# Performance work log

Hardware: AMD Instinct MI355X
Metric: run time of the kernel (lower is better)

## Reference

```python
import jax, jax.numpy as jnp
import numpy as np

N, C_IN, H, W = 16, 32, 512, 512
C_OUT, K, STRIDE = 32, 3, 1


def setup_inputs() -> dict:
    key = jax.random.key(0)
    k1, k2, k3 = jax.random.split(key, 3)
    x = jax.random.normal(k1, (N, C_IN, H, W), dtype=jnp.float32)
    weight = jax.random.normal(k2, (C_OUT, C_IN, K, K), dtype=jnp.float32) * 0.05
    bias = jax.random.normal(k3, (C_OUT,), dtype=jnp.float32) * 0.05
    return {"x": x, "weight": weight, "bias": bias}


def reference(x, weight, bias):
    # Direct 2D convolution, NCHW / OIHW, stride 1, no padding (VALID),
    # matching the module's per-pixel multiply+sum with padding=0.
    out = jax.lax.conv_general_dilated(
        x, weight,
        window_strides=(STRIDE, STRIDE),
        padding="VALID",
        dimension_numbers=("NCHW", "OIHW", "NCHW"),
    )
    return out + bias[None, :, None, None]
```

## Files before the change

### kernel.cpp

```cpp
#include <hip/hip_runtime.h>


namespace {
constexpr int NI    = 16;
constexpr int C_IN  = 32;
constexpr int HI    = 512;
constexpr int WI    = 512;
constexpr int C_OUT = 32;
constexpr int HO    = 510;
constexpr int WO    = 510;

constexpr int RT    = 6;
constexpr int PT    = 64;
constexpr int XROWS = RT + 2;
constexpr int XCOLS = PT + 2;
constexpr int PSTR  = 36;
constexpr int HIWI  = HI * WI;
}

typedef __attribute__((ext_vector_type(4))) float  floatx4;
typedef __attribute__((ext_vector_type(8))) __bf16 bf16x8;
typedef __attribute__((ext_vector_type(4))) __bf16 bf16x4;
typedef __attribute__((ext_vector_type(4))) unsigned short ushortx4;

__global__ void conv_wprep(const float* __restrict__ w, __bf16* __restrict__ ws) {
  const int t = threadIdx.x;
  for (int i = t; i < 9 * 2 * 64 * 8; i += 256) {
    const int j    = i & 7;
    const int lane = (i >> 3) & 63;
    const int h    = (i >> 9) & 1;
    const int tap  = i >> 10;
    const int co   = h * 16 + (lane & 15);
    const int ci   = (lane >> 4) * 8 + j;
    ws[i] = (__bf16)w[(co * C_IN + ci) * 9 + tap];
  }
}

__global__ __launch_bounds__(256, 4)
void conv3x3_mfma(const float* __restrict__ x, const __bf16* __restrict__ ws,
                  const float* __restrict__ bias, float* __restrict__ out) {
  __shared__ unsigned short lds[XROWS * XCOLS * PSTR];

  const int t    = threadIdx.x;
  const int lane = t & 63;
  const int wv   = t >> 6;
  const int quad = lane >> 4;
  const int l16  = lane & 15;

  const int x0 = blockIdx.x * PT;
  const int y0 = blockIdx.y * RT;
  const int n  = blockIdx.z;

  for (int p = t; p < XROWS * XCOLS; p += 256) {
    const int row = p / XCOLS;
    const int col = p - row * XCOLS;
    int gx = x0 + col;
    if (gx > WI - 1) gx = WI - 1;
    const float* xp = x + ((size_t)(n * C_IN) * HI + (y0 + row)) * WI + gx;
    union { __bf16 b[32]; ushortx4 q[8]; } pk;
#pragma unroll
    for (int ci = 0; ci < C_IN; ++ci)
      pk.b[ci] = (__bf16)xp[ci * HIWI];
    unsigned short* dst = &lds[p * PSTR];
#pragma unroll
    for (int k = 0; k < 8; ++k)
      *reinterpret_cast<ushortx4*>(dst + k * 4) = pk.q[k];
  }

  bf16x8 afrag[9][2];
#pragma unroll
  for (int tap = 0; tap < 9; ++tap)
#pragma unroll
    for (int h = 0; h < 2; ++h)
      afrag[tap][h] = *reinterpret_cast<const bf16x8*>(ws + ((tap * 2 + h) * 64 + lane) * 8);

  float b0[4], b1[4];
#pragma unroll
  for (int r = 0; r < 4; ++r) {
    b0[r] = bias[quad * 4 + r];
    b1[r] = bias[quad * 4 + r + 16];
  }

  __syncthreads();

  const int pbase  = wv * 16 + l16;
  const int px     = x0 + pbase;
  const bool valid = px < WO;

  for (int row = 0; row < RT; ++row) {
    floatx4 acc0 = {b0[0], b0[1], b0[2], b0[3]};
    floatx4 acc1 = {b1[0], b1[1], b1[2], b1[3]};
#pragma unroll
    for (int ky = 0; ky < 3; ++ky)
#pragma unroll
      for (int kx = 0; kx < 3; ++kx) {
        union { bf16x8 v; bf16x4 h[2]; } bf;
        const int base = ((row + ky) * XCOLS + pbase + kx) * PSTR + quad * 8;
        bf.h[0] = *reinterpret_cast<const bf16x4*>(&lds[base]);
        bf.h[1] = *reinterpret_cast<const bf16x4*>(&lds[base + 4]);
        acc0 = __builtin_amdgcn_mfma_f32_16x16x32_bf16(afrag[ky * 3 + kx][0], bf.v, acc0, 0, 0, 0);
        acc1 = __builtin_amdgcn_mfma_f32_16x16x32_bf16(afrag[ky * 3 + kx][1], bf.v, acc1, 0, 0, 0);
      }
    if (valid) {
      float* op = out + ((size_t)(n * C_OUT + quad * 4) * HO + (y0 + row)) * WO + px;
#pragma unroll
      for (int r = 0; r < 4; ++r) {
        op[r * (HO * WO)]        = acc0[r];
        op[(16 + r) * (HO * WO)] = acc1[r];
      }
    }
  }
}

extern "C" void kernel_launch(void* const* d_in, const int* in_sizes, int n_in,
                              void* d_out, int out_size, void* d_ws, size_t ws_size,
                              hipStream_t stream) {
  const float* x    = (const float*)d_in[0];
  const float* w    = (const float*)d_in[1];
  const float* bias = (const float*)d_in[2];
  float* out        = (float*)d_out;
  __bf16* ws        = (__bf16*)d_ws;

  conv_wprep<<<dim3(1), 256, 0, stream>>>(w, ws);

  dim3 grid(WI / PT, HO / RT, NI);
  conv3x3_mfma<<<grid, 256, 0, stream>>>(x, ws, bias, out);
}
```

Measured before the change: 1.001 ms.

## Split waves across output-channel halves and halve row tile for occupancy

Each wave now computes 16 output channels for 32 pixels instead of 32 channels for 16 pixels. This halves the per-wave A-fragment registers, and the launch bound is raised to allow more resident blocks. The row tile drops from 6 to 3, which shrinks LDS per block but raises the halo overhead (5 input rows loaded per 3 output rows) and doubles the number of blocks. Each wave also issues twice the B-fragment LDS reads per MFMA pair while reusing each A fragment twice.

```diff
diff --git a/kernel.cpp b/kernel.cpp
--- a/kernel.cpp
+++ b/kernel.cpp
@@ -10,7 +10,7 @@
 constexpr int HO    = 510;
 constexpr int WO    = 510;
 
-constexpr int RT    = 6;
+constexpr int RT    = 3;
 constexpr int PT    = 64;
 constexpr int XROWS = RT + 2;
 constexpr int XCOLS = PT + 2;
@@ -36,7 +36,7 @@
   }
 }
 
-__global__ __launch_bounds__(256, 4)
+__global__ __launch_bounds__(256, 6)
 void conv3x3_mfma(const float* __restrict__ x, const __bf16* __restrict__ ws,
                   const float* __restrict__ bias, float* __restrict__ out) {
   __shared__ unsigned short lds[XROWS * XCOLS * PSTR];
@@ -46,6 +46,8 @@
   const int wv   = t >> 6;
   const int quad = lane >> 4;
   const int l16  = lane & 15;
+  const int xh   = wv & 1;
+  const int ch   = wv >> 1;
 
   const int x0 = blockIdx.x * PT;
   const int y0 = blockIdx.y * RT;
@@ -67,47 +69,44 @@
       *reinterpret_cast<ushortx4*>(dst + k * 4) = pk.q[k];
   }
 
-  bf16x8 afrag[9][2];
+  bf16x8 afrag[9];
 #pragma unroll
   for (int tap = 0; tap < 9; ++tap)
+    afrag[tap] = *reinterpret_cast<const bf16x8*>(ws + ((tap * 2 + ch) * 64 + lane) * 8);
+
+  float bv[4];
 #pragma unroll
-    for (int h = 0; h < 2; ++h)
-      afrag[tap][h] = *reinterpret_cast<const bf16x8*>(ws + ((tap * 2 + h) * 64 + lane) * 8);
-
-  float b0[4], b1[4];
-#pragma unroll
-  for (int r = 0; r < 4; ++r) {
-    b0[r] = bias[quad * 4 + r];
-    b1[r] = bias[quad * 4 + r + 16];
-  }
+  for (int r = 0; r < 4; ++r)
+    bv[r] = bias[ch * 16 + quad * 4 + r];
 
   __syncthreads();
 
-  const int pbase  = wv * 16 + l16;
-  const int px     = x0 + pbase;
-  const bool valid = px < WO;
+  const int p0  = xh * 32 + l16;
+  const int px0 = x0 + p0;
+  const int px1 = px0 + 16;
+  const bool valid1 = px1 < WO;
 
   for (int row = 0; row < RT; ++row) {
-    floatx4 acc0 = {b0[0], b0[1], b0[2], b0[3]};
-    floatx4 acc1 = {b1[0], b1[1], b1[2], b1[3]};
+    floatx4 acc0 = {bv[0], bv[1], bv[2], bv[3]};
+    floatx4 acc1 = {bv[0], bv[1], bv[2], bv[3]};
 #pragma unroll
     for (int ky = 0; ky < 3; ++ky)
 #pragma unroll
       for (int kx = 0; kx < 3; ++kx) {
-        union { bf16x8 v; bf16x4 h[2]; } bf;
-        const int base = ((row + ky) * XCOLS + pbase + kx) * PSTR + quad * 8;
-        bf.h[0] = *reinterpret_cast<const bf16x4*>(&lds[base]);
-        bf.h[1] = *reinterpret_cast<const bf16x4*>(&lds[base + 4]);
-        acc0 = __builtin_amdgcn_mfma_f32_16x16x32_bf16(afrag[ky * 3 + kx][0], bf.v, acc0, 0, 0, 0);
-        acc1 = __builtin_amdgcn_mfma_f32_16x16x32_bf16(afrag[ky * 3 + kx][1], bf.v, acc1, 0, 0, 0);
+        const int base0 = ((row + ky) * XCOLS + p0 + kx) * PSTR + quad * 8;
+        union { bf16x8 v; bf16x4 h[2]; } bf0, bf1;
+        bf0.h[0] = *reinterpret_cast<const bf16x4*>(&lds[base0]);
+        bf0.h[1] = *reinterpret_cast<const bf16x4*>(&lds[base0 + 4]);
+        bf1.h[0] = *reinterpret_cast<const bf16x4*>(&lds[base0 + 16 * PSTR]);
+        bf1.h[1] = *reinterpret_cast<const bf16x4*>(&lds[base0 + 16 * PSTR + 4]);
+        acc0 = __builtin_amdgcn_mfma_f32_16x16x32_bf16(afrag[ky * 3 + kx], bf0.v, acc0, 0, 0, 0);
+        acc1 = __builtin_amdgcn_mfma_f32_16x16x32_bf16(afrag[ky * 3 + kx], bf1.v, acc1, 0, 0, 0);
       }
-    if (valid) {
-      float* op = out + ((size_t)(n * C_OUT + quad * 4) * HO + (y0 + row)) * WO + px;
+    float* op = out + ((size_t)(n * C_OUT + ch * 16 + quad * 4) * HO + (y0 + row)) * WO;
 #pragma unroll
-      for (int r = 0; r < 4; ++r) {
-        op[r * (HO * WO)]        = acc0[r];
-        op[(16 + r) * (HO * WO)] = acc1[r];
-      }
+    for (int r = 0; r < 4; ++r) {
+      op[r * (HO * WO) + px0] = acc0[r];
+      if (valid1) op[r * (HO * WO) + px1] = acc1[r];
     }
   }
 }
```

After: 1.420 ms. 41.8% more time.

## Split output channels across twice as many waves per block

Applied to the files above, without the earlier changes.

Doubles the block to 512 threads, so each wave computes 16 output channels for its 16-pixel strip instead of all 32. The LDS tile load is spread over more threads and each wave holds half the weight fragments, which lowers register pressure and adds waves for latency hiding. In exchange, each wave now reads the input fragments from LDS for only one MFMA, doubling LDS reads per MFMA.

```diff
diff --git a/kernel.cpp b/kernel.cpp
--- a/kernel.cpp
+++ b/kernel.cpp
@@ -16,6 +16,7 @@
 constexpr int XCOLS = PT + 2;
 constexpr int PSTR  = 36;
 constexpr int HIWI  = HI * WI;
+constexpr int NT    = 512;
 }
 
 typedef __attribute__((ext_vector_type(4))) float  floatx4;
@@ -36,7 +37,7 @@
   }
 }
 
-__global__ __launch_bounds__(256, 4)
+__global__ __launch_bounds__(NT, 8)
 void conv3x3_mfma(const float* __restrict__ x, const __bf16* __restrict__ ws,
                   const float* __restrict__ bias, float* __restrict__ out) {
   __shared__ unsigned short lds[XROWS * XCOLS * PSTR];
@@ -46,12 +47,14 @@
   const int wv   = t >> 6;
   const int quad = lane >> 4;
   const int l16  = lane & 15;
+  const int ch   = wv >> 2;
+  const int xq   = wv & 3;
 
   const int x0 = blockIdx.x * PT;
   const int y0 = blockIdx.y * RT;
   const int n  = blockIdx.z;
 
-  for (int p = t; p < XROWS * XCOLS; p += 256) {
+  for (int p = t; p < XROWS * XCOLS; p += NT) {
     const int row = p / XCOLS;
     const int col = p - row * XCOLS;
     int gx = x0 + col;
@@ -67,47 +70,39 @@
       *reinterpret_cast<ushortx4*>(dst + k * 4) = pk.q[k];
   }
 
-  bf16x8 afrag[9][2];
+  bf16x8 afrag[9];
 #pragma unroll
   for (int tap = 0; tap < 9; ++tap)
+    afrag[tap] = *reinterpret_cast<const bf16x8*>(ws + ((tap * 2 + ch) * 64 + lane) * 8);
+
+  float bv[4];
 #pragma unroll
-    for (int h = 0; h < 2; ++h)
-      afrag[tap][h] = *reinterpret_cast<const bf16x8*>(ws + ((tap * 2 + h) * 64 + lane) * 8);
-
-  float b0[4], b1[4];
-#pragma unroll
-  for (int r = 0; r < 4; ++r) {
-    b0[r] = bias[quad * 4 + r];
-    b1[r] = bias[quad * 4 + r + 16];
-  }
+  for (int r = 0; r < 4; ++r)
+    bv[r] = bias[ch * 16 + quad * 4 + r];
 
   __syncthreads();
 
-  const int pbase  = wv * 16 + l16;
-  const int px     = x0 + pbase;
+  const int p0  = xq * 16 + l16;
+  const int px  = x0 + p0;
   const bool valid = px < WO;
 
   for (int row = 0; row < RT; ++row) {
-    floatx4 acc0 = {b0[0], b0[1], b0[2], b0[3]};
-    floatx4 acc1 = {b1[0], b1[1], b1[2], b1[3]};
+    floatx4 acc = {bv[0], bv[1], bv[2], bv[3]};
 #pragma unroll
     for (int ky = 0; ky < 3; ++ky)
 #pragma unroll
       for (int kx = 0; kx < 3; ++kx) {
+        const int base = ((row + ky) * XCOLS + p0 + kx) * PSTR + quad * 8;
         union { bf16x8 v; bf16x4 h[2]; } bf;
-        const int base = ((row + ky) * XCOLS + pbase + kx) * PSTR + quad * 8;
         bf.h[0] = *reinterpret_cast<const bf16x4*>(&lds[base]);
         bf.h[1] = *reinterpret_cast<const bf16x4*>(&lds[base + 4]);
-        acc0 = __builtin_amdgcn_mfma_f32_16x16x32_bf16(afrag[ky * 3 + kx][0], bf.v, acc0, 0, 0, 0);
-        acc1 = __builtin_amdgcn_mfma_f32_16x16x32_bf16(afrag[ky * 3 + kx][1], bf.v, acc1, 0, 0, 0);
+        acc = __builtin_amdgcn_mfma_f32_16x16x32_bf16(afrag[ky * 3 + kx], bf.v, acc, 0, 0, 0);
       }
     if (valid) {
-      float* op = out + ((size_t)(n * C_OUT + quad * 4) * HO + (y0 + row)) * WO + px;
+      float* op = out + ((size_t)(n * C_OUT + ch * 16 + quad * 4) * HO + (y0 + row)) * WO + px;
 #pragma unroll
-      for (int r = 0; r < 4; ++r) {
-        op[r * (HO * WO)]        = acc0[r];
-        op[(16 + r) * (HO * WO)] = acc1[r];
-      }
+      for (int r = 0; r < 4; ++r)
+        op[r * (HO * WO)] = acc[r];
     }
   }
 }
@@ -124,5 +119,5 @@
   conv_wprep<<<dim3(1), 256, 0, stream>>>(w, ws);
 
   dim3 grid(WI / PT, HO / RT, NI);
-  conv3x3_mfma<<<grid, 256, 0, stream>>>(x, ws, bias, out);
+  conv3x3_mfma<<<grid, NT, 0, stream>>>(x, ws, bias, out);
 }
```

New measurement: 1.259 ms. 1.26x slower.

## Vectorize input tile staging with float4 loads, lane shuffles and prefetch

Applied to the files above, without the earlier changes.

Replaces the per-pixel scalar gather of 32 channels with float4 loads along x, where four lanes load four channels and transpose the 4x4 block via cross-lane shuffles before writing bf16 quads to LDS. Loads are software-pipelined six deep in registers, and the LDS tile is widened to 68 columns to match 17 float4 groups. Occupancy hint drops from 4 to 3 blocks per SM to make room for the extra prefetch registers. This aims to cut global load instruction count and improve coalescing, at the cost of shuffle ALU work and possibly lower occupancy.

```diff
diff --git a/kernel.cpp b/kernel.cpp
--- a/kernel.cpp
+++ b/kernel.cpp
@@ -13,9 +13,11 @@
 constexpr int RT    = 6;
 constexpr int PT    = 64;
 constexpr int XROWS = RT + 2;
-constexpr int XCOLS = PT + 2;
+constexpr int XCOLS = 68;
 constexpr int PSTR  = 36;
 constexpr int HIWI  = HI * WI;
+constexpr int NPASS = 17;
+constexpr int PDEPTH = 6;
 }
 
 typedef __attribute__((ext_vector_type(4))) float  floatx4;
@@ -36,35 +38,74 @@
   }
 }
 
-__global__ __launch_bounds__(256, 4)
+__global__ __launch_bounds__(256, 3)
 void conv3x3_mfma(const float* __restrict__ x, const __bf16* __restrict__ ws,
                   const float* __restrict__ bias, float* __restrict__ out) {
-  __shared__ unsigned short lds[XROWS * XCOLS * PSTR];
+  __shared__ __align__(16) unsigned short lds[XROWS * XCOLS * PSTR];
 
   const int t    = threadIdx.x;
   const int lane = t & 63;
   const int wv   = t >> 6;
   const int quad = lane >> 4;
   const int l16  = lane & 15;
+  const int q    = t & 3;
 
   const int x0 = blockIdx.x * PT;
   const int y0 = blockIdx.y * RT;
   const int n  = blockIdx.z;
 
-  for (int p = t; p < XROWS * XCOLS; p += 256) {
-    const int row = p / XCOLS;
-    const int col = p - row * XCOLS;
-    int gx = x0 + col;
-    if (gx > WI - 1) gx = WI - 1;
-    const float* xp = x + ((size_t)(n * C_IN) * HI + (y0 + row)) * WI + gx;
-    union { __bf16 b[32]; ushortx4 q[8]; } pk;
+  const float* xb = x + (size_t)n * C_IN * HIWI + (size_t)y0 * WI;
+
+  auto addr_of = [&](int p) -> const float* {
+    const int gid = p * 64 + (t >> 2);
+    const int x4  = gid % 17;
+    const int rc  = gid / 17;
+    const int c4  = rc & 7;
+    const int row = rc >> 3;
+    int gx = x0 + x4 * 4;
+    if (gx > WI - 4) gx = WI - 4;
+    return xb + (size_t)(c4 * 4 + q) * HIWI + row * WI + gx;
+  };
+
+  floatx4 vb[PDEPTH];
 #pragma unroll
-    for (int ci = 0; ci < C_IN; ++ci)
-      pk.b[ci] = (__bf16)xp[ci * HIWI];
-    unsigned short* dst = &lds[p * PSTR];
+  for (int p = 0; p < PDEPTH; ++p)
+    vb[p] = *reinterpret_cast<const floatx4*>(addr_of(p));
+
 #pragma unroll
-    for (int k = 0; k < 8; ++k)
-      *reinterpret_cast<ushortx4*>(dst + k * 4) = pk.q[k];
+  for (int p = 0; p < NPASS; ++p) {
+    const floatx4 v = vb[p % PDEPTH];
+    if (p + PDEPTH < NPASS)
+      vb[p % PDEPTH] = *reinterpret_cast<const floatx4*>(addr_of(p + PDEPTH));
+
+    const float sA = (q & 1) ? v.x : v.y;
+    const float rA = __shfl_xor(sA, 1);
+    const float a0 = (q & 1) ? rA : v.x;
+    const float a1 = (q & 1) ? v.y : rA;
+    const float sB = (q & 1) ? v.z : v.w;
+    const float rB = __shfl_xor(sB, 1);
+    const float a2 = (q & 1) ? rB : v.z;
+    const float a3 = (q & 1) ? v.w : rB;
+    const float sC = (q & 2) ? a0 : a2;
+    const float rC = __shfl_xor(sC, 2);
+    const float w0 = (q & 2) ? rC : a0;
+    const float w2 = (q & 2) ? a2 : rC;
+    const float sD = (q & 2) ? a1 : a3;
+    const float rD = __shfl_xor(sD, 2);
+    const float w1 = (q & 2) ? rD : a1;
+    const float w3 = (q & 2) ? a3 : rD;
+
+    const int gid = p * 64 + (t >> 2);
+    const int x4  = gid % 17;
+    const int rc  = gid / 17;
+    const int c4  = rc & 7;
+    const int row = rc >> 3;
+    const int px  = x4 * 4 + q;
+
+    union { __bf16 b[4]; ushortx4 u; } pk;
+    pk.b[0] = (__bf16)w0; pk.b[1] = (__bf16)w1;
+    pk.b[2] = (__bf16)w2; pk.b[3] = (__bf16)w3;
+    *reinterpret_cast<ushortx4*>(&lds[(row * XCOLS + px) * PSTR + c4 * 4]) = pk.u;
   }
 
   bf16x8 afrag[9][2];
```

New measurement: 1.015 ms. No clear change (+1.3%).
